# Optimization experiments

Hardware: AMD Instinct MI355X
Metric: run time of the kernel (lower is better)

The kernel has to match this reference:

```python
import jax, jax.numpy as jnp
import numpy as np

N, E = 50000, 800000
F_IN, F_EDGE = 64, 16
HEADS, C_HEAD = 4, 32
HC = HEADS * C_HEAD  # 128 = hidden_node_channels
MLP_IN = F_IN + HC   # 192
MLP0, MLP1 = 128, 128
NEG_SLOPE = 0.2


def leaky_relu(x):
    return jnp.where(x >= 0, x, NEG_SLOPE * x)


def layer_norm(x, g, b, eps=1e-5):
    mu = jnp.mean(x, axis=-1, keepdims=True)
    var = jnp.mean(jnp.square(x - mu), axis=-1, keepdims=True)
    return (x - mu) * jax.lax.rsqrt(var + eps) * g + b


def setup_inputs() -> dict:
    key = jax.random.key(0)
    ks = jax.random.split(key, 24)
    s = 0.05
    inp = {
        "node_features": jax.random.normal(ks[0], (N, F_IN), jnp.float32),
        "edge_features": jax.random.normal(ks[1], (E, F_EDGE), jnp.float32),
        "edge_index": jax.random.randint(ks[2], (2, E), 0, N, jnp.int32),
        # GATv2Conv params (share_weights=False, bias=True, edge_dim=16)
        "W_l": jax.random.normal(ks[3], (F_IN, HC), jnp.float32) * s,
        "b_l": jax.random.normal(ks[4], (HC,), jnp.float32) * s,
        "W_r": jax.random.normal(ks[5], (F_IN, HC), jnp.float32) * s,
        "b_r": jax.random.normal(ks[6], (HC,), jnp.float32) * s,
        "W_e": jax.random.normal(ks[7], (F_EDGE, HC), jnp.float32) * s,
        "att": jax.random.normal(ks[8], (HEADS, C_HEAD), jnp.float32) * s,
        "gat_bias": jax.random.normal(ks[9], (HC,), jnp.float32) * s,
        # residual_connection: Linear(64->128) + LayerNorm
        "res_W": jax.random.normal(ks[10], (F_IN, MLP1), jnp.float32) * s,
        "res_b": jax.random.normal(ks[11], (MLP1,), jnp.float32) * s,
        "res_g": 1.0 + jax.random.normal(ks[12], (MLP1,), jnp.float32) * s,
        "res_beta": jax.random.normal(ks[13], (MLP1,), jnp.float32) * s,
        # upd MLP: two ffn_blocks (Linear -> LayerNorm -> ReLU)
        "W0": jax.random.normal(ks[14], (MLP_IN, MLP0), jnp.float32) * s,
        "b0": jax.random.normal(ks[15], (MLP0,), jnp.float32) * s,
        "g0": 1.0 + jax.random.normal(ks[16], (MLP0,), jnp.float32) * s,
        "beta0": jax.random.normal(ks[17], (MLP0,), jnp.float32) * s,
        "W1": jax.random.normal(ks[18], (MLP0, MLP1), jnp.float32) * s,
        "b1": jax.random.normal(ks[19], (MLP1,), jnp.float32) * s,
        "g1": 1.0 + jax.random.normal(ks[20], (MLP1,), jnp.float32) * s,
        "beta1": jax.random.normal(ks[21], (MLP1,), jnp.float32) * s,
    }
    return inp


def reference(node_features, edge_features, edge_index,
              W_l, b_l, W_r, b_r, W_e, att, gat_bias,
              res_W, res_b, res_g, res_beta,
              W0, b0, g0, beta0, W1, b1, g1, beta1):
    src, dst = edge_index[0], edge_index[1]

    # ---- GATv2Conv ----
    x_l = (node_features @ W_l + b_l).reshape(N, HEADS, C_HEAD)  # source transform
    x_r = (node_features @ W_r + b_r).reshape(N, HEADS, C_HEAD)  # target transform
    e = (edge_features @ W_e).reshape(E, HEADS, C_HEAD)

    x_j = x_l[src]                      # [E,H,C] messages
    m = x_j + x_r[dst] + e              # [E,H,C]
    logits = jnp.sum(leaky_relu(m) * att, axis=-1)  # [E,H]

    # segment softmax over incoming edges of each destination node
    mx = jax.ops.segment_max(logits, dst, num_segments=N)      # [N,H]
    ex = jnp.exp(logits - mx[dst])                             # [E,H]
    den = jax.ops.segment_sum(ex, dst, num_segments=N)         # [N,H]
    alpha = ex / den[dst]                                      # [E,H]

    agg = jax.ops.segment_sum(alpha[..., None] * x_j, dst, num_segments=N)
    gat_out = agg.reshape(N, HC) + gat_bias                    # [N,128]

    # ---- residual concat-MLP ----
    identity = layer_norm(node_features @ res_W + res_b, res_g, res_beta)
    h = jnp.concatenate([node_features, gat_out], axis=-1)     # [N,192]
    h = jax.nn.relu(layer_norm(h @ W0 + b0, g0, beta0))
    h = jax.nn.relu(layer_norm(h @ W1 + b1, g1, beta1))
    return identity + h
```

## Files before the change

kernel.cpp:

```cpp
#include <hip/hip_runtime.h>

#define NN 50000
#define NE 800000
#define NB 196
#define K1B 782

typedef __attribute__((ext_vector_type(8))) short bf16x8;
typedef __attribute__((ext_vector_type(4))) float f32x4;
typedef __attribute__((ext_vector_type(2))) _Float16 h2f;

__device__ __forceinline__ int rfl(int v) { return __builtin_amdgcn_readfirstlane(v); }

__device__ __forceinline__ unsigned short bfb(float x) {
    union { float f; unsigned u; } v; v.f = x;
    unsigned r = v.u + 0x7FFFu + ((v.u >> 16) & 1u);
    return (unsigned short)(r >> 16);
}
__device__ __forceinline__ unsigned pkbf(float lo, float hi) {
    return ((unsigned)bfb(hi) << 16) | (unsigned)bfb(lo);
}
__device__ __forceinline__ unsigned pkh2(float a, float b) {
    union { h2f h; unsigned u; } x;
    x.h.x = (_Float16)a; x.h.y = (_Float16)b;
    return x.u;
}
__device__ __forceinline__ float fdot2u(unsigned a, unsigned b, float c) {
    union { unsigned u; h2f h; } ua, ub; ua.u = a; ub.u = b;
    return __builtin_amdgcn_fdot2(ua.h, ub.h, c, false);
}

__device__ __forceinline__ float dpp_reduce16(float p) {
    int t;
    t = __builtin_amdgcn_update_dpp(0, __float_as_int(p), 0xB1, 0xF, 0xF, false);
    p += __int_as_float(t);
    t = __builtin_amdgcn_update_dpp(0, __float_as_int(p), 0x4E, 0xF, 0xF, false);
    p += __int_as_float(t);
    t = __builtin_amdgcn_update_dpp(0, __float_as_int(p), 0x124, 0xF, 0xF, false);
    p += __int_as_float(t);
    t = __builtin_amdgcn_update_dpp(0, __float_as_int(p), 0x128, 0xF, 0xF, false);
    p += __int_as_float(t);
    return p;
}

__global__ __launch_bounds__(256) void k0_prep(
    const float* __restrict__ W_l, const float* __restrict__ W_r,
    const float* __restrict__ res_W, const float* __restrict__ W0,
    const float* __restrict__ W1, const float* __restrict__ W_e,
    const float* __restrict__ ef,
    unsigned short* __restrict__ Wtl, unsigned short* __restrict__ Wtr,
    unsigned short* __restrict__ Wtres, unsigned short* __restrict__ Wt0,
    unsigned short* __restrict__ Wt1,
    unsigned* __restrict__ Wep, unsigned* __restrict__ efp,
    int* __restrict__ deg, int* __restrict__ row_start)
{
    const int t0 = blockIdx.x * 256 + threadIdx.x;
    const int nth = gridDim.x * 256;
    for (int t = t0; t < NE * 8; t += nth) {
        float2 v = *(const float2*)(ef + 2 * t);
        efp[t] = pkh2(v.x, v.y);
    }
    if (t0 < 24576) { int n = t0 / 192, k = t0 - n * 192; Wt0[t0] = bfb(W0[k * 128 + n]); }
    if (t0 < 16384) { int n = t0 >> 7, k = t0 & 127; Wt1[t0] = bfb(W1[k * 128 + n]); }
    if (t0 < 8192) {
        int n = t0 >> 6, k = t0 & 63;
        Wtl[t0]   = bfb(W_l[k * 128 + n]);
        Wtr[t0]   = bfb(W_r[k * 128 + n]);
        Wtres[t0] = bfb(res_W[k * 128 + n]);
    }
    if (t0 < 1024) {
        int c = t0 >> 3, j = t0 & 7;
        Wep[t0] = pkh2(W_e[(2 * j) * 128 + c], W_e[(2 * j + 1) * 128 + c]);
    }
    if (t0 < NN) deg[t0] = 0;
    if (t0 == 0) row_start[NN] = NE;
}

__global__ __launch_bounds__(256, 4) void ka_nodes_degree(
    const float* __restrict__ nf,
    const unsigned short* __restrict__ Wtl, const float* __restrict__ b_l,
    const unsigned short* __restrict__ Wtr, const float* __restrict__ b_r,
    const unsigned short* __restrict__ Wtres, const float* __restrict__ res_b,
    const float* __restrict__ res_g, const float* __restrict__ res_beta,
    unsigned* __restrict__ xlp, float* __restrict__ x_r, float* __restrict__ ident,
    const int* __restrict__ eidx, int* __restrict__ deg, int* __restrict__ rank)
{
    if (blockIdx.x >= K1B) {
        int e = (blockIdx.x - K1B) * 256 + threadIdx.x;
        if (e < NE) rank[e] = atomicAdd(deg + eidx[NE + e], 1);
        return;
    }
    __shared__ __align__(16) unsigned As32[64 * 36];
    const int tid = threadIdx.x;
    const int node0 = blockIdx.x * 64;

    for (int i = tid; i < 64 * 32; i += 256) {
        int n = i >> 5, c2 = i & 31;
        int gn = node0 + n;
        float2 v = make_float2(0.f, 0.f);
        if (gn < NN) v = *(const float2*)(nf + gn * 64 + 2 * c2);
        As32[n * 36 + c2] = pkbf(v.x, v.y);
    }
    __syncthreads();

    const int lane = tid & 63, w = tid >> 6;
    const int c = lane & 15, ko = lane >> 4;
    const unsigned short* As = (const unsigned short*)As32;
    bf16x8 a0 = *(const bf16x8*)(As + (w * 16 + c) * 72 + 0 * 32 + ko * 8);
    bf16x8 a1 = *(const bf16x8*)(As + (w * 16 + c) * 72 + 1 * 32 + ko * 8);
    const int lrow0 = node0 + w * 16 + 4 * ko;

    #pragma unroll
    for (int p = 0; p < 3; ++p) {
        const unsigned short* Wt = (p == 0) ? Wtl : (p == 1) ? Wtr : Wtres;
        f32x4 acc[8];
        #pragma unroll
        for (int nt = 0; nt < 8; ++nt) acc[nt] = f32x4{0.f, 0.f, 0.f, 0.f};
        #pragma unroll
        for (int nt = 0; nt < 8; ++nt) {
            bf16x8 bf0 = *(const bf16x8*)(Wt + (nt * 16 + c) * 64 + 0 * 32 + ko * 8);
            acc[nt] = __builtin_amdgcn_mfma_f32_16x16x32_bf16(a0, bf0, acc[nt], 0, 0, 0);
            bf16x8 bf1 = *(const bf16x8*)(Wt + (nt * 16 + c) * 64 + 1 * 32 + ko * 8);
            acc[nt] = __builtin_amdgcn_mfma_f32_16x16x32_bf16(a1, bf1, acc[nt], 0, 0, 0);
        }
        if (p == 0) {
            float bv[8];
            #pragma unroll
            for (int nt = 0; nt < 8; ++nt) bv[nt] = b_l[nt * 16 + c];
            #pragma unroll
            for (int reg = 0; reg < 4; ++reg) {
                int row = lrow0 + reg;
                #pragma unroll
                for (int nt = 0; nt < 8; ++nt) {
                    float v = acc[nt][reg] + bv[nt];
                    float v2 = __shfl_xor(v, 1, 64);
                    if (row < NN && (lane & 1) == 0)
                        xlp[row * 64 + nt * 8 + (c >> 1)] = pkh2(v, v2);
                }
            }
        } else if (p == 1) {
            float bv[8];
            #pragma unroll
            for (int nt = 0; nt < 8; ++nt) bv[nt] = b_r[nt * 16 + c];
            #pragma unroll
            for (int reg = 0; reg < 4; ++reg) {
                int row = lrow0 + reg;
                if (row < NN) {
                    #pragma unroll
                    for (int nt = 0; nt < 8; ++nt)
                        x_r[row * 128 + nt * 16 + c] = acc[nt][reg] + bv[nt];
                }
            }
        } else {
            float bv[8], gv[8], tv[8];
            #pragma unroll
            for (int nt = 0; nt < 8; ++nt) {
                bv[nt] = res_b[nt * 16 + c];
                gv[nt] = res_g[nt * 16 + c];
                tv[nt] = res_beta[nt * 16 + c];
            }
            #pragma unroll
            for (int reg = 0; reg < 4; ++reg) {
                float sum = 0.f, sq = 0.f, hv[8];
                #pragma unroll
                for (int nt = 0; nt < 8; ++nt) {
                    float v = acc[nt][reg] + bv[nt];
                    hv[nt] = v; sum += v; sq += v * v;
                }
                #pragma unroll
                for (int m = 1; m <= 8; m <<= 1) {
                    sum += __shfl_xor(sum, m, 64);
                    sq  += __shfl_xor(sq, m, 64);
                }
                float mean = sum * (1.f / 128.f);
                float inv  = rsqrtf(sq * (1.f / 128.f) - mean * mean + 1e-5f);
                int row = lrow0 + reg;
                if (row < NN) {
                    #pragma unroll
                    for (int nt = 0; nt < 8; ++nt)
                        ident[row * 128 + nt * 16 + c] =
                            (hv[nt] - mean) * inv * gv[nt] + tv[nt];
                }
            }
        }
    }
}

__global__ __launch_bounds__(256) void k3a_blocksum(
    const int* __restrict__ deg, int* __restrict__ bsum)
{
    __shared__ int ws[4];
    int i = blockIdx.x * 256 + threadIdx.x;
    int v = (i < NN) ? deg[i] : 0;
    #pragma unroll
    for (int m = 32; m >= 1; m >>= 1) v += __shfl_xor(v, m, 64);
    if ((threadIdx.x & 63) == 0) ws[threadIdx.x >> 6] = v;
    __syncthreads();
    if (threadIdx.x == 0) bsum[blockIdx.x] = ws[0] + ws[1] + ws[2] + ws[3];
}

__global__ __launch_bounds__(256) void k3c_apply(
    const int* __restrict__ deg, const int* __restrict__ bsum,
    int* __restrict__ row_start)
{
    __shared__ int wsum[4];
    __shared__ int roff[4];
    const int tid = threadIdx.x, lane = tid & 63, wid = tid >> 6;
    int bv = (tid < blockIdx.x) ? bsum[tid] : 0;
    #pragma unroll
    for (int m = 32; m >= 1; m >>= 1) bv += __shfl_xor(bv, m, 64);
    if (lane == 0) roff[wid] = bv;

    int i = blockIdx.x * 256 + tid;
    int v = (i < NN) ? deg[i] : 0;
    int sc = v;
    #pragma unroll
    for (int m = 1; m < 64; m <<= 1) {
        int t = __shfl_up(sc, m, 64);
        if (lane >= m) sc += t;
    }
    if (lane == 63) wsum[wid] = sc;
    __syncthreads();
    int off = roff[0] + roff[1] + roff[2] + roff[3];
    for (int w = 0; w < wid; ++w) off += wsum[w];
    int excl = off + sc - v;
    if (i < NN) row_start[i] = excl;
}

__global__ __launch_bounds__(256) void k4_scatter(
    const int* __restrict__ eidx, const int* __restrict__ row_start,
    const int* __restrict__ rank, int2* __restrict__ csr_es)
{
    int e = blockIdx.x * 256 + threadIdx.x;
    if (e >= NE) return;
    int dst = eidx[NE + e];
    csr_es[row_start[dst] + rank[e]] = make_int2(e, eidx[e]);
}

__global__ __launch_bounds__(256, 4) void k5_attn_aggregate(
    const int2* __restrict__ csr_es, const int* __restrict__ row_start,
    const unsigned* __restrict__ efp, const unsigned* __restrict__ Wep,
    const float* __restrict__ att,
    const unsigned* __restrict__ xlp, const float* __restrict__ x_r,
    const float* __restrict__ gat_bias,
    float* __restrict__ gat_out)
{
    const int lane = threadIdx.x & 63;
    const int node = (blockIdx.x * 256 + threadIdx.x) >> 6;
    if (node >= NN) return;
    const int c = lane * 2;

    uint4 t0 = *(const uint4*)(Wep + c * 8);
    uint4 t1 = *(const uint4*)(Wep + c * 8 + 4);
    uint4 t2 = *(const uint4*)(Wep + (c + 1) * 8);
    uint4 t3 = *(const uint4*)(Wep + (c + 1) * 8 + 4);
    unsigned wx0 = t0.x, wx1 = t0.y, wx2 = t0.z, wx3 = t0.w;
    unsigned wx4 = t1.x, wx5 = t1.y, wx6 = t1.z, wx7 = t1.w;
    unsigned wy0 = t2.x, wy1 = t2.y, wy2 = t2.z, wy3 = t2.w;
    unsigned wy4 = t3.x, wy5 = t3.y, wy6 = t3.z, wy7 = t3.w;

    const float2 a2 = *(const float2*)(att + c);
    const float2 xr = *(const float2*)(x_r + node * 128 + c);
    const uint4* __restrict__ efq = (const uint4*)efp;
    const unsigned* __restrict__ xlc = xlp + lane;

    const int sj  = rfl(row_start[node]);
    const int epj = rfl(row_start[node + 1]);

    float den = 0.f, n0 = 0.f, n1 = 0.f;

    if (sj < epj) {
        const int last = epj - 1;
        uint4 aE0, aE1, bE0, bE1, cE0, cE1;
        unsigned aX, bX, cX;

#define LOADS(E0_, E1_, X_, IDX_)                                          \
        { int jc = (IDX_); if (jc > last) jc = last;                       \
          int2 es = csr_es[jc];                                            \
          int eid = rfl(es.x), srcn = rfl(es.y);                           \
          E0_ = efq[eid * 2 + 0]; E1_ = efq[eid * 2 + 1];                  \
          X_  = xlc[srcn * 64]; }

#define CONSUME(E0_, E1_, X_)                                              \
        { asm volatile("" : "+v"(wx0), "+v"(wx1), "+v"(wx2), "+v"(wx3),    \
                            "+v"(wx4), "+v"(wx5), "+v"(wx6), "+v"(wx7));   \
          asm volatile("" : "+v"(wy0), "+v"(wy1), "+v"(wy2), "+v"(wy3),    \
                            "+v"(wy4), "+v"(wy5), "+v"(wy6), "+v"(wy7));   \
          union { unsigned u; h2f h; } ux; ux.u = (X_);                    \
          float cx0 = (float)ux.h.x, cx1 = (float)ux.h.y;                  \
          float ax = cx0 + xr.x;                                           \
          float ay = cx1 + xr.y;                                           \
          float bx = 0.f, by = 0.f;                                        \
          ax = fdot2u((E0_).x, wx0, ax);  ay = fdot2u((E0_).x, wy0, ay);   \
          bx = fdot2u((E0_).y, wx1, bx);  by = fdot2u((E0_).y, wy1, by);   \
          ax = fdot2u((E0_).z, wx2, ax);  ay = fdot2u((E0_).z, wy2, ay);   \
          bx = fdot2u((E0_).w, wx3, bx);  by = fdot2u((E0_).w, wy3, by);   \
          ax = fdot2u((E1_).x, wx4, ax);  ay = fdot2u((E1_).x, wy4, ay);   \
          bx = fdot2u((E1_).y, wx5, bx);  by = fdot2u((E1_).y, wy5, by);   \
          ax = fdot2u((E1_).z, wx6, ax);  ay = fdot2u((E1_).z, wy6, ay);   \
          bx = fdot2u((E1_).w, wx7, bx);  by = fdot2u((E1_).w, wy7, by);   \
          float evx = ax + bx;                                             \
          float evy = ay + by;                                             \
          float lx = fmaxf(evx, 0.2f * evx);                               \
          float ly = fmaxf(evy, 0.2f * evy);                               \
          float p = lx * a2.x + ly * a2.y;                                 \
          p = dpp_reduce16(p);                                             \
          float ev = __expf(p);                                            \
          den += ev; n0 += ev * cx0; n1 += ev * cx1; }

        LOADS(aE0, aE1, aX, sj);
        LOADS(bE0, bE1, bX, sj + 1);
        int j = sj;
        while (j + 3 <= epj) {
            LOADS(cE0, cE1, cX, j + 2);
            CONSUME(aE0, aE1, aX);
            LOADS(aE0, aE1, aX, j + 3);
            CONSUME(bE0, bE1, bX);
            LOADS(bE0, bE1, bX, j + 4);
            CONSUME(cE0, cE1, cX);
            j += 3;
        }
        if (j < epj)     CONSUME(aE0, aE1, aX);
        if (j + 1 < epj) CONSUME(bE0, bE1, bX);
#undef LOADS
#undef CONSUME
    }
    float rden = (den > 0.f) ? (1.f / den) : 0.f;
    float2 gb = *(const float2*)(gat_bias + c);
    float2 o; o.x = n0 * rden + gb.x; o.y = n1 * rden + gb.y;
    *(float2*)(gat_out + node * 128 + c) = o;
}

__global__ __launch_bounds__(256, 4) void k6_mlp_mfma(
    const float* __restrict__ nf, const float* __restrict__ gat,
    const float* __restrict__ ident,
    const unsigned short* __restrict__ Wt0, const float* __restrict__ b0,
    const float* __restrict__ g0, const float* __restrict__ be0,
    const unsigned short* __restrict__ Wt1, const float* __restrict__ b1,
    const float* __restrict__ g1, const float* __restrict__ be1,
    float* __restrict__ out)
{
    __shared__ __align__(16) unsigned LDS[64 * 100];
    const int tid = threadIdx.x;
    const int node0 = blockIdx.x * 64;

    for (int i = tid; i < 64 * 96; i += 256) {
        int n = i / 96, c2 = i - n * 96;
        int gn = node0 + n;
        float2 v = make_float2(0.f, 0.f);
        if (gn < NN)
            v = (c2 < 32) ? *(const float2*)(nf + gn * 64 + 2 * c2)
                          : *(const float2*)(gat + gn * 128 + 2 * (c2 - 32));
        LDS[n * 100 + c2] = pkbf(v.x, v.y);
    }
    __syncthreads();

    const int lane = tid & 63, w = tid >> 6;
    const int c = lane & 15, ko = lane >> 4;
    const int lrow = w * 16 + 4 * ko;

    f32x4 acc[8];
    #pragma unroll
    for (int nt = 0; nt < 8; ++nt) acc[nt] = f32x4{0.f, 0.f, 0.f, 0.f};

    #pragma unroll
    for (int kb = 0; kb < 6; ++kb) {
        bf16x8 a = *(const bf16x8*)((const unsigned short*)LDS +
                                    (w * 16 + c) * 200 + kb * 32 + ko * 8);
        #pragma unroll
        for (int nt = 0; nt < 8; ++nt) {
            bf16x8 b = *(const bf16x8*)(Wt0 + (nt * 16 + c) * 192 + kb * 32 + ko * 8);
            acc[nt] = __builtin_amdgcn_mfma_f32_16x16x32_bf16(a, b, acc[nt], 0, 0, 0);
        }
    }

    float bv[8], gv[8], tv[8];
    #pragma unroll
    for (int nt = 0; nt < 8; ++nt) {
        bv[nt] = b0[nt * 16 + c];
        gv[nt] = g0[nt * 16 + c];
        tv[nt] = be0[nt * 16 + c];
    }
    __syncthreads();

    unsigned short* Hs = (unsigned short*)LDS;
    #pragma unroll
    for (int reg = 0; reg < 4; ++reg) {
        float sum = 0.f, sq = 0.f, hv[8];
        #pragma unroll
        for (int nt = 0; nt < 8; ++nt) {
            float v = acc[nt][reg] + bv[nt];
            hv[nt] = v; sum += v; sq += v * v;
        }
        #pragma unroll
        for (int m = 1; m <= 8; m <<= 1) {
            sum += __shfl_xor(sum, m, 64);
            sq  += __shfl_xor(sq, m, 64);
        }
        float mean = sum * (1.f / 128.f);
        float inv  = rsqrtf(sq * (1.f / 128.f) - mean * mean + 1e-5f);
        #pragma unroll
        for (int nt = 0; nt < 8; ++nt) {
            float h = fmaxf((hv[nt] - mean) * inv * gv[nt] + tv[nt], 0.f);
            Hs[(lrow + reg) * 136 + nt * 16 + c] = bfb(h);
        }
    }
    __syncthreads();

    #pragma unroll
    for (int nt = 0; nt < 8; ++nt) acc[nt] = f32x4{0.f, 0.f, 0.f, 0.f};
    #pragma unroll
    for (int kb = 0; kb < 4; ++kb) {
        bf16x8 a = *(const bf16x8*)((const unsigned short*)LDS +
                                    (w * 16 + c) * 136 + kb * 32 + ko * 8);
        #pragma unroll
        for (int nt = 0; nt < 8; ++nt) {
            bf16x8 b = *(const bf16x8*)(Wt1 + (nt * 16 + c) * 128 + kb * 32 + ko * 8);
            acc[nt] = __builtin_amdgcn_mfma_f32_16x16x32_bf16(a, b, acc[nt], 0, 0, 0);
        }
    }

    #pragma unroll
    for (int nt = 0; nt < 8; ++nt) {
        bv[nt] = b1[nt * 16 + c];
        gv[nt] = g1[nt * 16 + c];
        tv[nt] = be1[nt * 16 + c];
    }
    #pragma unroll
    for (int reg = 0; reg < 4; ++reg) {
        float sum = 0.f, sq = 0.f, hv[8];
        #pragma unroll
        for (int nt = 0; nt < 8; ++nt) {
            float v = acc[nt][reg] + bv[nt];
            hv[nt] = v; sum += v; sq += v * v;
        }
        #pragma unroll
        for (int m = 1; m <= 8; m <<= 1) {
            sum += __shfl_xor(sum, m, 64);
            sq  += __shfl_xor(sq, m, 64);
        }
        float mean = sum * (1.f / 128.f);
        float inv  = rsqrtf(sq * (1.f / 128.f) - mean * mean + 1e-5f);
        int row = node0 + lrow + reg;
        if (row < NN) {
            #pragma unroll
            for (int nt = 0; nt < 8; ++nt) {
                float h = fmaxf((hv[nt] - mean) * inv * gv[nt] + tv[nt], 0.f);
                int col = nt * 16 + c;
                out[row * 128 + col] = ident[row * 128 + col] + h;
            }
        }
    }
}

extern "C" void kernel_launch(void* const* d_in, const int* in_sizes, int n_in,
                              void* d_out, int out_size, void* d_ws, size_t ws_size,
                              hipStream_t stream)
{
    const float* nf       = (const float*)d_in[0];
    const float* ef       = (const float*)d_in[1];
    const int*   eidx     = (const int*)d_in[2];
    const float* W_l      = (const float*)d_in[3];
    const float* b_l      = (const float*)d_in[4];
    const float* W_r      = (const float*)d_in[5];
    const float* b_r      = (const float*)d_in[6];
    const float* W_e      = (const float*)d_in[7];
    const float* att      = (const float*)d_in[8];
    const float* gat_bias = (const float*)d_in[9];
    const float* res_W    = (const float*)d_in[10];
    const float* res_b    = (const float*)d_in[11];
    const float* res_g    = (const float*)d_in[12];
    const float* res_beta = (const float*)d_in[13];
    const float* W0       = (const float*)d_in[14];
    const float* b0       = (const float*)d_in[15];
    const float* g0       = (const float*)d_in[16];
    const float* beta0    = (const float*)d_in[17];
    const float* W1       = (const float*)d_in[18];
    const float* b1       = (const float*)d_in[19];
    const float* g1       = (const float*)d_in[20];
    const float* beta1    = (const float*)d_in[21];
    float* out = (float*)d_out;

    char* ws = (char*)d_ws;
    size_t off = 0;
    auto alloc = [&](size_t bytes) -> void* {
        void* p = ws + off;
        off += (bytes + 255) & ~(size_t)255;
        return p;
    };
    unsigned* xlp  = (unsigned*)alloc((size_t)NN * 64 * 4);
    float* x_r     = (float*)alloc((size_t)NN * 128 * 4);
    float* ident   = (float*)alloc((size_t)NN * 128 * 4);
    int* deg       = (int*)alloc((size_t)NN * 4);
    int* row_start = (int*)alloc((size_t)(NN + 1) * 4);
    int* rank      = (int*)alloc((size_t)NE * 4);
    int* bsum      = (int*)alloc((size_t)(NB + 1) * 4);
    int2* csr_es   = (int2*)alloc((size_t)NE * 8);
    float* gat_out = (float*)alloc((size_t)NN * 128 * 4);
    unsigned short* Wtl   = (unsigned short*)alloc(8192 * 2);
    unsigned short* Wtr   = (unsigned short*)alloc(8192 * 2);
    unsigned short* Wtres = (unsigned short*)alloc(8192 * 2);
    unsigned short* Wt0   = (unsigned short*)alloc(24576 * 2);
    unsigned short* Wt1   = (unsigned short*)alloc(16384 * 2);
    unsigned* Wep = (unsigned*)alloc(1024 * 4);
    unsigned* efp = (unsigned*)alloc((size_t)NE * 8 * 4);

    k0_prep<<<8192, 256, 0, stream>>>(W_l, W_r, res_W, W0, W1, W_e, ef,
                                      Wtl, Wtr, Wtres, Wt0, Wt1, Wep, efp,
                                      deg, row_start);

    ka_nodes_degree<<<K1B + (NE + 255) / 256, 256, 0, stream>>>(
        nf, Wtl, b_l, Wtr, b_r, Wtres, res_b, res_g, res_beta,
        xlp, x_r, ident, eidx, deg, rank);

    k3a_blocksum<<<NB, 256, 0, stream>>>(deg, bsum);
    k3c_apply<<<NB, 256, 0, stream>>>(deg, bsum, row_start);

    k4_scatter<<<(NE + 255) / 256, 256, 0, stream>>>(eidx, row_start, rank, csr_es);

    k5_attn_aggregate<<<(NN * 64 + 255) / 256, 256, 0, stream>>>(
        csr_es, row_start, efp, Wep, att, xlp, x_r, gat_bias, gat_out);

    k6_mlp_mfma<<<(NN + 63) / 64, 256, 0, stream>>>(
        nf, gat_out, ident, Wt0, b0, g0, beta0, Wt1, b1, g1, beta1, out);
}
```

Measured before the change: 342.2 us.

## Batch CSR index loads per wave, deepen prefetch to 4, use hardware exp2

The per-node attention aggregation kernel now loads up to 64 CSR (edge id, source) pairs at once, one per lane, and pulls each with readlane, instead of issuing a scalar-broadcast load for every edge. The software pipeline of gathers goes from three to four buffers to hide more memory latency. The exp is replaced by raw v_exp_f32, with log2(e) folded into the attention vector. The deeper pipeline costs extra registers, and dropping the max subtraction (already absent before) still leaves a risk of overflow.

New measurement: 336.1 us. No clear change (-1.8%).

```diff
diff --git a/kernel.cpp b/kernel.cpp
--- a/kernel.cpp
+++ b/kernel.cpp
@@ -40,6 +40,12 @@
     t = __builtin_amdgcn_update_dpp(0, __float_as_int(p), 0x128, 0xF, 0xF, false);
     p += __int_as_float(t);
     return p;
+}
+
+__device__ __forceinline__ float exp2_hw(float x) {
+    float r;
+    asm("v_exp_f32 %0, %1" : "=v"(r) : "v"(x));
+    return r;
 }
 
 __global__ __launch_bounds__(256) void k0_prep(
@@ -258,7 +264,9 @@
     unsigned wy0 = t2.x, wy1 = t2.y, wy2 = t2.z, wy3 = t2.w;
     unsigned wy4 = t3.x, wy5 = t3.y, wy6 = t3.z, wy7 = t3.w;
 
-    const float2 a2 = *(const float2*)(att + c);
+    const float LOG2E = 1.44269504088896340736f;
+    float2 a2 = *(const float2*)(att + c);
+    a2.x *= LOG2E; a2.y *= LOG2E;
     const float2 xr = *(const float2*)(x_r + node * 128 + c);
     const uint4* __restrict__ efq = (const uint4*)efp;
     const unsigned* __restrict__ xlc = xlp + lane;
@@ -268,15 +276,18 @@
 
     float den = 0.f, n0 = 0.f, n1 = 0.f;
 
-    if (sj < epj) {
-        const int last = epj - 1;
-        uint4 aE0, aE1, bE0, bE1, cE0, cE1;
-        unsigned aX, bX, cX;
-
-#define LOADS(E0_, E1_, X_, IDX_)                                          \
-        { int jc = (IDX_); if (jc > last) jc = last;                       \
-          int2 es = csr_es[jc];                                            \
-          int eid = rfl(es.x), srcn = rfl(es.y);                           \
+    for (int base = sj; base < epj; base += 64) {
+        const int cnt = min(64, epj - base);
+        int pidx = base + lane; if (pidx > NE - 1) pidx = NE - 1;
+        const int2 mc = csr_es[pidx];
+
+        uint4 aE0, aE1, bE0, bE1, cE0, cE1, dE0, dE1;
+        unsigned aX, bX, cX, dX;
+
+#define LOADS(E0_, E1_, X_, K_)                                            \
+        { int kk = (K_); if (kk >= cnt) kk = cnt - 1;                      \
+          int eid  = __builtin_amdgcn_readlane(mc.x, kk);                  \
+          int srcn = __builtin_amdgcn_readlane(mc.y, kk);                  \
           E0_ = efq[eid * 2 + 0]; E1_ = efq[eid * 2 + 1];                  \
           X_  = xlc[srcn * 64]; }
 
@@ -304,23 +315,27 @@
           float ly = fmaxf(evy, 0.2f * evy);                               \
           float p = lx * a2.x + ly * a2.y;                                 \
           p = dpp_reduce16(p);                                             \
-          float ev = __expf(p);                                            \
+          float ev = exp2_hw(p);                                           \
           den += ev; n0 += ev * cx0; n1 += ev * cx1; }
 
-        LOADS(aE0, aE1, aX, sj);
-        LOADS(bE0, bE1, bX, sj + 1);
-        int j = sj;
-        while (j + 3 <= epj) {
-            LOADS(cE0, cE1, cX, j + 2);
+        LOADS(aE0, aE1, aX, 0);
+        LOADS(bE0, bE1, bX, 1);
+        LOADS(cE0, cE1, cX, 2);
+        int j = 0;
+        while (j + 4 <= cnt) {
+            LOADS(dE0, dE1, dX, j + 3);
             CONSUME(aE0, aE1, aX);
-            LOADS(aE0, aE1, aX, j + 3);
+            LOADS(aE0, aE1, aX, j + 4);
             CONSUME(bE0, bE1, bX);
-            LOADS(bE0, bE1, bX, j + 4);
+            LOADS(bE0, bE1, bX, j + 5);
             CONSUME(cE0, cE1, cX);
-            j += 3;
-        }
-        if (j < epj)     CONSUME(aE0, aE1, aX);
-        if (j + 1 < epj) CONSUME(bE0, bE1, bX);
+            LOADS(cE0, cE1, cX, j + 6);
+            CONSUME(dE0, dE1, dX);
+            j += 4;
+        }
+        if (j < cnt)     CONSUME(aE0, aE1, aX);
+        if (j + 1 < cnt) CONSUME(bE0, bE1, bX);
+        if (j + 2 < cnt) CONSUME(cE0, cE1, cX);
 #undef LOADS
 #undef CONSUME
     }
```
